# Performance work log

Hardware: AMD Instinct MI355X
Metric: run time of the kernel (lower is better)

## Reference

```python
import jax, jax.numpy as jnp
import numpy as np

NH = 16   # n_heads
HD = 64   # head_size
EMB = 1024  # n_embd = NH * HD
B, T = 4, 2048


def setup_inputs() -> dict:
    key = jax.random.key(0)
    k1, k2, k3 = jax.random.split(key, 3)
    x = jax.random.normal(k1, (B, T, EMB), dtype=jnp.float32)
    # torch Linear(in, out, bias=False): weight [out,in]; we store transposed [in,out]
    W_attn = jax.random.normal(k2, (EMB, 3 * NH * HD), dtype=jnp.float32) * (EMB ** -0.5)
    W_proj = jax.random.normal(k3, (NH * HD, EMB), dtype=jnp.float32) * ((NH * HD) ** -0.5)
    b_proj = jnp.zeros((EMB,), dtype=jnp.float32)
    return {"x": x, "W_attn": W_attn, "W_proj": W_proj, "b_proj": b_proj}


def reference(x, W_attn, W_proj, b_proj):
    Bq, Tq, C = x.shape
    qkv = x @ W_attn                      # [B,T,3*Nh*H]
    qs, ks, vs = jnp.split(qkv, 3, axis=2)
    def to_heads(t):                      # [B,T,Nh*H] -> [B,Nh,T,H]
        return t.reshape(Bq, Tq, NH, HD).transpose(0, 2, 1, 3)
    q, k, v = to_heads(qs), to_heads(ks), to_heads(vs)
    scores = jnp.einsum('bnth,bnsh->bnts', q, k) * (HD ** -0.5)  # [B,Nh,T,T]
    causal = jnp.tril(jnp.ones((Tq, Tq), dtype=bool))
    scores = jnp.where(causal, scores, -jnp.inf)
    attn = jax.nn.softmax(scores, axis=-1)
    # dropout is identity in eval mode
    y = jnp.einsum('bnts,bnsh->bnth', attn, v)                   # [B,Nh,T,H]
    y = y.transpose(0, 2, 1, 3).reshape(Bq, Tq, NH * HD)
    return y @ W_proj + b_proj
```

## Files before the change

kernel.cpp:

```cpp
#include <hip/hip_runtime.h>
#include <hip/hip_bf16.h>

#define NH 16
#define HD 64
#define EMB 1024
#define BB 4
#define TT 2048
#define MTOT (BB*TT)
#define N1 (3*NH*HD)
#define KD EMB

#define QSCALE 0.18033688011112042f
#define FMAX 14.0f

typedef __bf16 bf16x8 __attribute__((ext_vector_type(8)));
typedef __bf16 bf16x4 __attribute__((ext_vector_type(4)));
typedef float  f32x4  __attribute__((ext_vector_type(4)));
typedef __hip_bfloat16 hbf;

__device__ __forceinline__ void async_copy16(const hbf* g, hbf* l) {
    __builtin_amdgcn_global_load_lds(
        (const __attribute__((address_space(1))) void*)g,
        (__attribute__((address_space(3))) void*)l, 16, 0, 0);
}

__device__ __forceinline__ bf16x4 pack4(float x0, float x1, float x2, float x3) {
    union { bf16x4 v; hbf a[4]; } u;
    u.a[0] = __float2bfloat16(x0);
    u.a[1] = __float2bfloat16(x1);
    u.a[2] = __float2bfloat16(x2);
    u.a[3] = __float2bfloat16(x3);
    return u.v;
}


__global__ __launch_bounds__(256) void f32_to_bf16_v4(const float* __restrict__ in,
                                                      hbf* __restrict__ out, int n4) {
    int i = blockIdx.x * blockDim.x + threadIdx.x;
    if (i < n4) {
        float4 v = ((const float4*)in)[i];
        *(bf16x4*)(out + 4 * (size_t)i) = pack4(v.x, v.y, v.z, v.w);
    }
}

__global__ __launch_bounds__(256) void f32_to_bf16_T(const float* __restrict__ in,
                                                     hbf* __restrict__ out, int R, int C) {
    __shared__ float T[64][65];
    int bc = blockIdx.x % (C / 64), br = blockIdx.x / (C / 64);
    int r0 = br * 64, c0 = bc * 64;
    int tr = threadIdx.x >> 6, tc = threadIdx.x & 63;
    #pragma unroll
    for (int i = 0; i < 16; ++i)
        T[4 * i + tr][tc] = in[(size_t)(r0 + 4 * i + tr) * C + c0 + tc];
    __syncthreads();
    #pragma unroll
    for (int i = 0; i < 16; ++i)
        out[(size_t)(c0 + 4 * i + tr) * R + r0 + tc] = __float2bfloat16(T[tc][4 * i + tr]);
}


template<int NBN, int MODE>
__global__ __launch_bounds__(512, 4) void gemm8(
    const hbf* __restrict__ A, const hbf* __restrict__ Bt,
    hbf* __restrict__ qh, hbf* __restrict__ kh, hbf* __restrict__ vt,
    const float* __restrict__ bias, float* __restrict__ out)
{
    constexpr int NKT = KD / 64;
    __shared__ __align__(16) hbf As[2 * 128 * 64];
    __shared__ __align__(16) hbf Bs[2 * 128 * 64];

    int tid = threadIdx.x;
    int wv = tid >> 6, lane = tid & 63;
    int g = lane >> 4, c = lane & 15;
    int wm = wv >> 2, wn = wv & 3;
    int bn = blockIdx.x % NBN, bm = blockIdx.x / NBN;
    int m0 = bm * 128, n0 = bn * 128;

    int sr0 = tid >> 3;
    int sgc = (tid & 7) ^ (sr0 & 7);
    const hbf* Asrc0 = A  + (size_t)(m0 + sr0) * KD + sgc * 8;
    const hbf* Asrc1 = A  + (size_t)(m0 + 64 + sr0) * KD + sgc * 8;
    const hbf* Bsrc0 = Bt + (size_t)(n0 + sr0) * KD + sgc * 8;
    const hbf* Bsrc1 = Bt + (size_t)(n0 + 64 + sr0) * KD + sgc * 8;
    int ldst0 = (tid & ~63) * 8;
    int ldst1 = 4096 + (tid & ~63) * 8;

#define STAGE_A8(tt, buf) { async_copy16(Asrc0 + (tt) * 64, As + (buf) * 8192 + ldst0); \
                            async_copy16(Asrc1 + (tt) * 64, As + (buf) * 8192 + ldst1); }
#define STAGE_B8(tt, buf) { async_copy16(Bsrc0 + (tt) * 64, Bs + (buf) * 8192 + ldst0); \
                            async_copy16(Bsrc1 + (tt) * 64, Bs + (buf) * 8192 + ldst1); }

    int xr = c & 7;
    int aoff0 = (wm * 64 + c) * 64 + ((g ^ xr) << 3);
    int aoff1 = (wm * 64 + c) * 64 + (((4 + g) ^ xr) << 3);
    int boff0 = (wn * 32 + c) * 64 + ((g ^ xr) << 3);
    int boff1 = (wn * 32 + c) * 64 + (((4 + g) ^ xr) << 3);

    f32x4 acc[4][2];
    #pragma unroll
    for (int i = 0; i < 4; ++i)
        #pragma unroll
        for (int j = 0; j < 2; ++j) acc[i][j] = (f32x4){0.f, 0.f, 0.f, 0.f};

    STAGE_A8(0, 0);
    STAGE_B8(0, 0);
    STAGE_A8(1, 1);
    asm volatile("s_waitcnt vmcnt(2)" ::: "memory");
    asm volatile("s_barrier" ::: "memory");
    __builtin_amdgcn_sched_barrier(0);

    for (int t = 0; t < NKT; ++t) {
        int cur = t & 1;
        const hbf* Ab = As + cur * 8192;
        const hbf* Bb = Bs + cur * 8192;
        bf16x8 af[4][2], bfr[2];
        #pragma unroll
        for (int i = 0; i < 4; ++i) {
            af[i][0] = *(const bf16x8*)(Ab + aoff0 + i * 1024);
            af[i][1] = *(const bf16x8*)(Ab + aoff1 + i * 1024);
        }
        bfr[0] = *(const bf16x8*)(Bb + boff0);
        bfr[1] = *(const bf16x8*)(Bb + boff1);
        if (t + 1 < NKT) STAGE_B8(t + 1, cur ^ 1);
        __builtin_amdgcn_s_setprio(1);
        #pragma unroll
        for (int i = 0; i < 4; ++i) {
            acc[i][0] = __builtin_amdgcn_mfma_f32_16x16x32_bf16(af[i][0], bfr[0], acc[i][0], 0, 0, 0);
            acc[i][0] = __builtin_amdgcn_mfma_f32_16x16x32_bf16(af[i][1], bfr[1], acc[i][0], 0, 0, 0);
        }
        __builtin_amdgcn_s_setprio(0);
        asm volatile("s_barrier" ::: "memory");
        __builtin_amdgcn_sched_barrier(0);
        bfr[0] = *(const bf16x8*)(Bb + boff0 + 1024);
        bfr[1] = *(const bf16x8*)(Bb + boff1 + 1024);
        if (t + 2 < NKT) STAGE_A8(t + 2, cur);
        __builtin_amdgcn_s_setprio(1);
        #pragma unroll
        for (int i = 0; i < 4; ++i) {
            acc[i][1] = __builtin_amdgcn_mfma_f32_16x16x32_bf16(af[i][0], bfr[0], acc[i][1], 0, 0, 0);
            acc[i][1] = __builtin_amdgcn_mfma_f32_16x16x32_bf16(af[i][1], bfr[1], acc[i][1], 0, 0, 0);
        }
        __builtin_amdgcn_s_setprio(0);
        if (t + 2 < NKT) { asm volatile("s_waitcnt vmcnt(2)" ::: "memory"); }
        else             { asm volatile("s_waitcnt vmcnt(0)" ::: "memory"); }
        asm volatile("s_barrier" ::: "memory");
        __builtin_amdgcn_sched_barrier(0);
    }

#undef STAGE_A8
#undef STAGE_B8

    if constexpr (MODE == 0) {
        int colbase = n0 + wn * 32;
        int which = colbase >> 10;
        int h = (colbase & 1023) >> 6;
        int dbase = colbase & 63;
        int b = m0 / TT;
        int trow = (m0 % TT) + wm * 64;
        if (which < 2) {
            float scale = (which == 0) ? QSCALE : 1.0f;
            hbf* dst = ((which == 0) ? qh : kh) + ((size_t)b * NH + h) * TT * HD;
            #pragma unroll
            for (int i = 0; i < 4; ++i)
                #pragma unroll
                for (int nf = 0; nf < 2; ++nf) {
                    int d = dbase + nf * 16 + c;
                    #pragma unroll
                    for (int r = 0; r < 4; ++r) {
                        int trw = trow + i * 16 + g * 4 + r;
                        dst[(size_t)trw * HD + d] = __float2bfloat16(acc[i][nf][r] * scale);
                    }
                }
        } else {
            hbf* dst = vt + ((size_t)b * NH + h) * TT * HD;
            #pragma unroll
            for (int i = 0; i < 4; ++i)
                #pragma unroll
                for (int nf = 0; nf < 2; ++nf) {
                    int d = dbase + nf * 16 + c;
                    #pragma unroll
                    for (int r = 0; r < 4; ++r) {
                        int trw = trow + i * 16 + g * 4 + r;
                        dst[(size_t)d * TT + trw] = __float2bfloat16(acc[i][nf][r]);
                    }
                }
        }
    } else {
        #pragma unroll
        for (int i = 0; i < 4; ++i)
            #pragma unroll
            for (int nf = 0; nf < 2; ++nf) {
                int col = n0 + wn * 32 + nf * 16 + c;
                float bv = bias[col];
                #pragma unroll
                for (int r = 0; r < 4; ++r) {
                    int row = m0 + wm * 64 + i * 16 + g * 4 + r;
                    out[(size_t)row * EMB + col] = acc[i][nf][r] + bv;
                }
            }
    }
}


__global__ __launch_bounds__(512, 4) void attn(
    const hbf* __restrict__ qh, const hbf* __restrict__ kh, const hbf* __restrict__ vt,
    hbf* __restrict__ y)
{
    __shared__ __align__(16) hbf Ks[128 * 64];
    __shared__ __align__(16) hbf Vs[64 * 128];
    __shared__ __align__(16) hbf Ps[8][16 * 64];

    int tid = threadIdx.x;
    int wv = tid >> 6, lane = tid & 63;
    int g = lane >> 4, c = lane & 15;
    int c7 = c & 7;

    int bh = blockIdx.x >> 3;
    int pi = blockIdx.x & 7;
    int b = bh >> 4, h = bh & 15;

    const hbf* Q = qh + (size_t)bh * TT * HD;
    const hbf* K = kh + (size_t)bh * TT * HD;
    const hbf* V = vt + (size_t)bh * TT * HD;
    hbf* Pq = &Ps[wv][0];

    union { bf16x8 v; hbf a[8]; } uo;
    #pragma unroll
    for (int i = 0; i < 8; ++i) uo.a[i] = __float2bfloat16(1.0f);
    const bf16x8 ones8 = uo.v;

    #pragma unroll
    for (int pass = 0; pass < 2; ++pass) {
        int sst = pass ? (15 - pi) : pi;
        int qb = sst * 128;
        int q0 = qb + wv * 16;
        int kend = q0 + 16;
        int kmax = qb + 128;

        bf16x8 aq0 = *(const bf16x8*)(Q + (size_t)(q0 + c) * HD + g * 8);
        bf16x8 aq1 = *(const bf16x8*)(Q + (size_t)(q0 + c) * HD + 32 + g * 8);

        f32x4 lacc = (f32x4){0.f, 0.f, 0.f, 0.f};
        f32x4 o[4];
        #pragma unroll
        for (int d = 0; d < 4; ++d) o[d] = (f32x4){0.f, 0.f, 0.f, 0.f};

        for (int k0 = 0; k0 < kmax; k0 += 128) {
            __syncthreads();
            #pragma unroll
            for (int it = 0; it < 2; ++it) {
                int e = it * 4096 + tid * 8;
                int key = e >> 6, sblk = (e >> 3) & 7;
                int dblk = sblk ^ (key & 7);
                async_copy16(K + (size_t)(k0 + key) * HD + dblk * 8,
                             Ks + it * 4096 + (tid & ~63) * 8);
            }
            #pragma unroll
            for (int it = 0; it < 2; ++it) {
                int e = it * 4096 + tid * 8;
                int dim = e >> 7, kb = (e >> 3) & 15;
                int skb = kb ^ (dim & 7);
                async_copy16(V + (size_t)dim * TT + k0 + skb * 8,
                             Vs + it * 4096 + (tid & ~63) * 8);
            }
            __syncthreads();

            #pragma unroll
            for (int ch = 0; ch < 2; ++ch) {
                int c64 = k0 + ch * 64;
                if (c64 < kend) {
                    f32x4 s[4];
                    #pragma unroll
                    for (int t = 0; t < 4; ++t) {
                        int kt = c64 + 16 * t;
                        if (kt < kend) {
                            int rb = (ch * 64 + 16 * t + c) * 64;
                            bf16x8 kf0 = *(const bf16x8*)(Ks + rb + ((g ^ c7) << 3));
                            bf16x8 kf1 = *(const bf16x8*)(Ks + rb + (((4 + g) ^ c7) << 3));
                            f32x4 a = (f32x4){-FMAX, -FMAX, -FMAX, -FMAX};
                            a = __builtin_amdgcn_mfma_f32_16x16x32_bf16(kf0, aq0, a, 0, 0, 0);
                            a = __builtin_amdgcn_mfma_f32_16x16x32_bf16(kf1, aq1, a, 0, 0, 0);
                            if (kt == q0) {
                                #pragma unroll
                                for (int r = 0; r < 4; ++r)
                                    a[r] = (g * 4 + r <= c) ? a[r] : -1e30f;
                            }
                            s[t] = a;
                        } else
                            s[t] = (f32x4){-1e30f, -1e30f, -1e30f, -1e30f};
                    }
                    #pragma unroll
                    for (int t = 0; t < 4; ++t) {
                        f32x4 e;
                        #pragma unroll
                        for (int r = 0; r < 4; ++r) e[r] = __builtin_amdgcn_exp2f(s[t][r]);
                        *(bf16x4*)(Pq + c * 64 + (((2 * t + (g >> 1)) ^ c7) << 3) + ((g & 1) << 2)) =
                            pack4(e[0], e[1], e[2], e[3]);
                    }
                    #pragma unroll
                    for (int sc = 0; sc < 2; ++sc) {
                        if (c64 + 32 * sc < kend) {
                            bf16x8 pf = *(const bf16x8*)(Pq + c * 64 + (((4 * sc + g) ^ c7) << 3));
                            lacc = __builtin_amdgcn_mfma_f32_16x16x32_bf16(ones8, pf, lacc, 0, 0, 0);
                            #pragma unroll
                            for (int d = 0; d < 4; ++d) {
                                int dim = d * 16 + c;
                                bf16x8 vf = *(const bf16x8*)(Vs + dim * 128 +
                                              (((ch * 8 + 4 * sc + g) ^ c7) << 3));
                                o[d] = __builtin_amdgcn_mfma_f32_16x16x32_bf16(vf, pf, o[d], 0, 0, 0);
                            }
                        }
                    }
                }
            }
        }

        float inv = 1.0f / lacc[0];
        #pragma unroll
        for (int d = 0; d < 4; ++d) {
            *(bf16x4*)(y + (size_t)(b * TT + q0 + c) * EMB + h * HD + d * 16 + g * 4) =
                pack4(o[d][0] * inv, o[d][1] * inv, o[d][2] * inv, o[d][3] * inv);
        }
    }
}


extern "C" void kernel_launch(void* const* d_in, const int* in_sizes, int n_in,
                              void* d_out, int out_size, void* d_ws, size_t ws_size,
                              hipStream_t stream)
{
    const float* x      = (const float*)d_in[0];
    const float* W_attn = (const float*)d_in[1];
    const float* W_proj = (const float*)d_in[2];
    const float* b_proj = (const float*)d_in[3];
    float* out = (float*)d_out;

    char* ws = (char*)d_ws;
    hbf* xb    = (hbf*)ws; ws += (size_t)MTOT * KD * 2;
    hbf* wab_t = (hbf*)ws; ws += (size_t)N1 * KD * 2;
    hbf* wpb_t = (hbf*)ws; ws += (size_t)EMB * EMB * 2;
    hbf* qh    = (hbf*)ws; ws += (size_t)MTOT * EMB * 2;
    hbf* kh    = (hbf*)ws; ws += (size_t)MTOT * EMB * 2;
    hbf* vt    = (hbf*)ws; ws += (size_t)MTOT * EMB * 2;
    hbf* yb    = (hbf*)ws; ws += (size_t)MTOT * EMB * 2;

    f32_to_bf16_v4<<<(MTOT * KD / 4 + 255) / 256, 256, 0, stream>>>(x, xb, MTOT * KD / 4);
    f32_to_bf16_T<<<(KD / 64) * (N1 / 64), 256, 0, stream>>>(W_attn, wab_t, KD, N1);
    f32_to_bf16_T<<<(KD / 64) * (EMB / 64), 256, 0, stream>>>(W_proj, wpb_t, KD, EMB);

    gemm8<N1 / 128, 0><<<(MTOT / 128) * (N1 / 128), 512, 0, stream>>>(
        xb, wab_t, qh, kh, vt, nullptr, nullptr);
    attn<<<BB * NH * 8, 512, 0, stream>>>(qh, kh, vt, yb);
    gemm8<EMB / 128, 1><<<(MTOT / 128) * (EMB / 128), 512, 0, stream>>>(
        yb, wpb_t, nullptr, nullptr, nullptr, b_proj, out);
}
```

Measured before the change: 254.2 us.

## Use 256x256 GEMM tiles with ping-pong pipeline and remap block indices

The bf16 GEMM kernels are rewritten to compute 256x256 output tiles per workgroup instead of 128x128. The K loop is restructured into a quarter-tile schedule that interleaves LDS fragment loads, async global-to-LDS staging and MFMA bursts, with explicit barriers and double buffering. Block indices are remapped (XCD-aware) for both the GEMMs and the attention kernel to improve L2 locality. The aim is more data reuse per loaded byte and better overlap of memory with compute. In exchange the kernel uses more LDS and registers per workgroup (occupancy hint reduced to 2) and launches fewer workgroups.

```diff
diff --git a/kernel.cpp b/kernel.cpp
--- a/kernel.cpp
+++ b/kernel.cpp
@@ -59,145 +59,182 @@
 }
 
 
+#define GBAR  asm volatile("s_barrier" ::: "memory")
+#define GLGKM { asm volatile("s_waitcnt lgkmcnt(0)" ::: "memory"); __builtin_amdgcn_sched_barrier(0); }
+
 template<int NBN, int MODE>
-__global__ __launch_bounds__(512, 4) void gemm8(
+__global__ __launch_bounds__(512, 2) void gemm8p(
     const hbf* __restrict__ A, const hbf* __restrict__ Bt,
     hbf* __restrict__ qh, hbf* __restrict__ kh, hbf* __restrict__ vt,
     const float* __restrict__ bias, float* __restrict__ out)
 {
     constexpr int NKT = KD / 64;
-    __shared__ __align__(16) hbf As[2 * 128 * 64];
-    __shared__ __align__(16) hbf Bs[2 * 128 * 64];
+    constexpr int NIT = NKT / 2;
+    constexpr int GRID = (MTOT / 256) * NBN;
+    __shared__ __align__(16) hbf As[2 * 2 * 8192];
+    __shared__ __align__(16) hbf Bs[2 * 2 * 8192];
 
     int tid = threadIdx.x;
     int wv = tid >> 6, lane = tid & 63;
     int g = lane >> 4, c = lane & 15;
     int wm = wv >> 2, wn = wv & 3;
-    int bn = blockIdx.x % NBN, bm = blockIdx.x / NBN;
-    int m0 = bm * 128, n0 = bn * 128;
-
-    int sr0 = tid >> 3;
-    int sgc = (tid & 7) ^ (sr0 & 7);
-    const hbf* Asrc0 = A  + (size_t)(m0 + sr0) * KD + sgc * 8;
-    const hbf* Asrc1 = A  + (size_t)(m0 + 64 + sr0) * KD + sgc * 8;
-    const hbf* Bsrc0 = Bt + (size_t)(n0 + sr0) * KD + sgc * 8;
-    const hbf* Bsrc1 = Bt + (size_t)(n0 + 64 + sr0) * KD + sgc * 8;
-    int ldst0 = (tid & ~63) * 8;
-    int ldst1 = 4096 + (tid & ~63) * 8;
-
-#define STAGE_A8(tt, buf) { async_copy16(Asrc0 + (tt) * 64, As + (buf) * 8192 + ldst0); \
-                            async_copy16(Asrc1 + (tt) * 64, As + (buf) * 8192 + ldst1); }
-#define STAGE_B8(tt, buf) { async_copy16(Bsrc0 + (tt) * 64, Bs + (buf) * 8192 + ldst0); \
-                            async_copy16(Bsrc1 + (tt) * 64, Bs + (buf) * 8192 + ldst1); }
-
     int xr = c & 7;
-    int aoff0 = (wm * 64 + c) * 64 + ((g ^ xr) << 3);
-    int aoff1 = (wm * 64 + c) * 64 + (((4 + g) ^ xr) << 3);
-    int boff0 = (wn * 32 + c) * 64 + ((g ^ xr) << 3);
-    int boff1 = (wn * 32 + c) * 64 + (((4 + g) ^ xr) << 3);
-
-    f32x4 acc[4][2];
-    #pragma unroll
-    for (int i = 0; i < 4; ++i)
+    int wg = (blockIdx.x & 7) * (GRID / 8) + (blockIdx.x >> 3);
+    int bn = wg % NBN, bm = wg / NBN;
+    int m0 = bm * 256, n0 = bn * 256;
+
+    int r0 = tid >> 3;
+    int gc = (tid & 7) ^ (r0 & 7);
+    const hbf* pA = A  + (size_t)(m0 + r0) * KD + gc * 8;
+    const hbf* pB = Bt + (size_t)(n0 + r0) * KD + gc * 8;
+    int ldsd = (tid & ~63) * 8;
+
+#define STG_A(t, buf, hf) { \
+    async_copy16(pA + (size_t)((hf)*128     ) * KD + (t)*64, As + (buf)*16384 + (hf)*8192 + ldsd); \
+    async_copy16(pA + (size_t)((hf)*128 + 64) * KD + (t)*64, As + (buf)*16384 + (hf)*8192 + 4096 + ldsd); }
+#define STG_B(t, buf, hf) { \
+    async_copy16(pB + (size_t)((hf)*128     ) * KD + (t)*64, Bs + (buf)*16384 + (hf)*8192 + ldsd); \
+    async_copy16(pB + (size_t)((hf)*128 + 64) * KD + (t)*64, Bs + (buf)*16384 + (hf)*8192 + 4096 + ldsd); }
+
+    bf16x8 af[4][2];
+    bf16x8 bfr[2][2][2];
+    f32x4 acc[2][2][4][2];
+    #pragma unroll
+    for (int a0 = 0; a0 < 2; ++a0)
+      #pragma unroll
+      for (int a1 = 0; a1 < 2; ++a1)
         #pragma unroll
-        for (int j = 0; j < 2; ++j) acc[i][j] = (f32x4){0.f, 0.f, 0.f, 0.f};
-
-    STAGE_A8(0, 0);
-    STAGE_B8(0, 0);
-    STAGE_A8(1, 1);
-    asm volatile("s_waitcnt vmcnt(2)" ::: "memory");
-    asm volatile("s_barrier" ::: "memory");
+        for (int a2 = 0; a2 < 4; ++a2)
+          #pragma unroll
+          for (int a3 = 0; a3 < 2; ++a3) acc[a0][a1][a2][a3] = (f32x4){0.f,0.f,0.f,0.f};
+
+#define LDA(buf, mh) { _Pragma("unroll") for (int mi = 0; mi < 4; ++mi) { \
+    const hbf* ap = As + (buf)*16384 + wm*8192 + ((mh)*64 + mi*16 + c)*64; \
+    af[mi][0] = *(const bf16x8*)(ap + ((g ^ xr) << 3)); \
+    af[mi][1] = *(const bf16x8*)(ap + (((4 + g) ^ xr) << 3)); } }
+#define LDB(buf, nq) { _Pragma("unroll") for (int ni = 0; ni < 2; ++ni) { \
+    const hbf* bp = Bs + (buf)*16384 + (wn >> 1)*8192 + ((wn & 1)*64 + (nq)*32 + ni*16 + c)*64; \
+    bfr[nq][ni][0] = *(const bf16x8*)(bp + ((g ^ xr) << 3)); \
+    bfr[nq][ni][1] = *(const bf16x8*)(bp + (((4 + g) ^ xr) << 3)); } }
+#define MM(mh, nq) { __builtin_amdgcn_s_setprio(1); \
+    _Pragma("unroll") for (int mi = 0; mi < 4; ++mi) \
+      _Pragma("unroll") for (int ni = 0; ni < 2; ++ni) { \
+        acc[mh][nq][mi][ni] = __builtin_amdgcn_mfma_f32_16x16x32_bf16(af[mi][0], bfr[nq][ni][0], acc[mh][nq][mi][ni], 0, 0, 0); \
+        acc[mh][nq][mi][ni] = __builtin_amdgcn_mfma_f32_16x16x32_bf16(af[mi][1], bfr[nq][ni][1], acc[mh][nq][mi][ni], 0, 0, 0); } \
+    __builtin_amdgcn_s_setprio(0); }
+
+    STG_A(0, 0, 0); STG_A(0, 0, 1); STG_B(0, 0, 0); STG_B(0, 0, 1);
+    STG_B(1, 1, 0); STG_B(1, 1, 1);
+    asm volatile("s_waitcnt vmcnt(4)" ::: "memory");
+    GBAR;
     __builtin_amdgcn_sched_barrier(0);
 
-    for (int t = 0; t < NKT; ++t) {
-        int cur = t & 1;
-        const hbf* Ab = As + cur * 8192;
-        const hbf* Bb = Bs + cur * 8192;
-        bf16x8 af[4][2], bfr[2];
-        #pragma unroll
-        for (int i = 0; i < 4; ++i) {
-            af[i][0] = *(const bf16x8*)(Ab + aoff0 + i * 1024);
-            af[i][1] = *(const bf16x8*)(Ab + aoff1 + i * 1024);
-        }
-        bfr[0] = *(const bf16x8*)(Bb + boff0);
-        bfr[1] = *(const bf16x8*)(Bb + boff1);
-        if (t + 1 < NKT) STAGE_B8(t + 1, cur ^ 1);
-        __builtin_amdgcn_s_setprio(1);
-        #pragma unroll
-        for (int i = 0; i < 4; ++i) {
-            acc[i][0] = __builtin_amdgcn_mfma_f32_16x16x32_bf16(af[i][0], bfr[0], acc[i][0], 0, 0, 0);
-            acc[i][0] = __builtin_amdgcn_mfma_f32_16x16x32_bf16(af[i][1], bfr[1], acc[i][0], 0, 0, 0);
-        }
-        __builtin_amdgcn_s_setprio(0);
-        asm volatile("s_barrier" ::: "memory");
+    for (int i = 0; i < NIT - 1; ++i) {
+        LDA(0, 0); LDB(0, 0); STG_A(2*i+1, 1, 0);
+        GBAR; GLGKM; MM(0, 0); GBAR;
+        LDB(0, 1); STG_A(2*i+1, 1, 1);
+        GBAR; GLGKM; MM(0, 1); GBAR;
+        LDA(0, 1); STG_B(2*i+2, 0, 0);
+        GBAR; GLGKM; MM(1, 0); GBAR;
+        STG_B(2*i+2, 0, 1);
+        GBAR; MM(1, 1);
+        asm volatile("s_waitcnt vmcnt(4)" ::: "memory");
+        GBAR;
+        LDA(1, 0); LDB(1, 0); STG_A(2*i+2, 0, 0);
+        GBAR; GLGKM; MM(0, 0); GBAR;
+        LDB(1, 1); STG_A(2*i+2, 0, 1);
+        GBAR; GLGKM; MM(0, 1); GBAR;
+        LDA(1, 1); STG_B(2*i+3, 1, 0);
+        GBAR; GLGKM; MM(1, 0); GBAR;
+        STG_B(2*i+3, 1, 1);
+        GBAR; MM(1, 1);
+        asm volatile("s_waitcnt vmcnt(4)" ::: "memory");
+        GBAR;
         __builtin_amdgcn_sched_barrier(0);
-        bfr[0] = *(const bf16x8*)(Bb + boff0 + 1024);
-        bfr[1] = *(const bf16x8*)(Bb + boff1 + 1024);
-        if (t + 2 < NKT) STAGE_A8(t + 2, cur);
-        __builtin_amdgcn_s_setprio(1);
-        #pragma unroll
-        for (int i = 0; i < 4; ++i) {
-            acc[i][1] = __builtin_amdgcn_mfma_f32_16x16x32_bf16(af[i][0], bfr[0], acc[i][1], 0, 0, 0);
-            acc[i][1] = __builtin_amdgcn_mfma_f32_16x16x32_bf16(af[i][1], bfr[1], acc[i][1], 0, 0, 0);
-        }
-        __builtin_amdgcn_s_setprio(0);
-        if (t + 2 < NKT) { asm volatile("s_waitcnt vmcnt(2)" ::: "memory"); }
-        else             { asm volatile("s_waitcnt vmcnt(0)" ::: "memory"); }
-        asm volatile("s_barrier" ::: "memory");
-        __builtin_amdgcn_sched_barrier(0);
-    }
-
-#undef STAGE_A8
-#undef STAGE_B8
+    }
+    {
+        LDA(0, 0); LDB(0, 0); STG_A(NKT-1, 1, 0);
+        GBAR; GLGKM; MM(0, 0); GBAR;
+        LDB(0, 1); STG_A(NKT-1, 1, 1);
+        GBAR; GLGKM; MM(0, 1); GBAR;
+        LDA(0, 1);
+        GBAR; GLGKM; MM(1, 0); GBAR;
+        MM(1, 1);
+        asm volatile("s_waitcnt vmcnt(0)" ::: "memory");
+        GBAR;
+        LDA(1, 0); LDB(1, 0);
+        GBAR; GLGKM; MM(0, 0); GBAR;
+        LDB(1, 1);
+        GBAR; GLGKM; MM(0, 1); GBAR;
+        LDA(1, 1);
+        GBAR; GLGKM; MM(1, 0); GBAR;
+        MM(1, 1);
+    }
+#undef STG_A
+#undef STG_B
+#undef LDA
+#undef LDB
+#undef MM
 
     if constexpr (MODE == 0) {
-        int colbase = n0 + wn * 32;
+        int colbase = n0 + wn * 64;
         int which = colbase >> 10;
         int h = (colbase & 1023) >> 6;
-        int dbase = colbase & 63;
         int b = m0 / TT;
-        int trow = (m0 % TT) + wm * 64;
+        int trow0 = (m0 % TT) + wm * 128;
         if (which < 2) {
             float scale = (which == 0) ? QSCALE : 1.0f;
             hbf* dst = ((which == 0) ? qh : kh) + ((size_t)b * NH + h) * TT * HD;
             #pragma unroll
-            for (int i = 0; i < 4; ++i)
+            for (int mh = 0; mh < 2; ++mh)
+              #pragma unroll
+              for (int mi = 0; mi < 4; ++mi)
                 #pragma unroll
-                for (int nf = 0; nf < 2; ++nf) {
-                    int d = dbase + nf * 16 + c;
-                    #pragma unroll
-                    for (int r = 0; r < 4; ++r) {
-                        int trw = trow + i * 16 + g * 4 + r;
-                        dst[(size_t)trw * HD + d] = __float2bfloat16(acc[i][nf][r] * scale);
-                    }
-                }
+                for (int nq = 0; nq < 2; ++nq)
+                  #pragma unroll
+                  for (int ni = 0; ni < 2; ++ni) {
+                      int d = nq * 32 + ni * 16 + c;
+                      #pragma unroll
+                      for (int r = 0; r < 4; ++r) {
+                          int t = trow0 + mh * 64 + mi * 16 + g * 4 + r;
+                          dst[(size_t)t * HD + d] = __float2bfloat16(acc[mh][nq][mi][ni][r] * scale);
+                      }
+                  }
         } else {
             hbf* dst = vt + ((size_t)b * NH + h) * TT * HD;
             #pragma unroll
-            for (int i = 0; i < 4; ++i)
+            for (int mh = 0; mh < 2; ++mh)
+              #pragma unroll
+              for (int mi = 0; mi < 4; ++mi)
                 #pragma unroll
-                for (int nf = 0; nf < 2; ++nf) {
-                    int d = dbase + nf * 16 + c;
-                    #pragma unroll
-                    for (int r = 0; r < 4; ++r) {
-                        int trw = trow + i * 16 + g * 4 + r;
-                        dst[(size_t)d * TT + trw] = __float2bfloat16(acc[i][nf][r]);
-                    }
-                }
+                for (int nq = 0; nq < 2; ++nq)
+                  #pragma unroll
+                  for (int ni = 0; ni < 2; ++ni) {
+                      int d = nq * 32 + ni * 16 + c;
+                      #pragma unroll
+                      for (int r = 0; r < 4; ++r) {
+                          int t = trow0 + mh * 64 + mi * 16 + g * 4 + r;
+                          dst[(size_t)d * TT + t] = __float2bfloat16(acc[mh][nq][mi][ni][r]);
+                      }
+                  }
         }
     } else {
         #pragma unroll
-        for (int i = 0; i < 4; ++i)
-            #pragma unroll
-            for (int nf = 0; nf < 2; ++nf) {
-                int col = n0 + wn * 32 + nf * 16 + c;
-                float bv = bias[col];
-                #pragma unroll
-                for (int r = 0; r < 4; ++r) {
-                    int row = m0 + wm * 64 + i * 16 + g * 4 + r;
-                    out[(size_t)row * EMB + col] = acc[i][nf][r] + bv;
-                }
-            }
+        for (int mh = 0; mh < 2; ++mh)
+          #pragma unroll
+          for (int mi = 0; mi < 4; ++mi)
+            #pragma unroll
+            for (int nq = 0; nq < 2; ++nq)
+              #pragma unroll
+              for (int ni = 0; ni < 2; ++ni) {
+                  int col = n0 + wn * 64 + nq * 32 + ni * 16 + c;
+                  float bv = bias[col];
+                  #pragma unroll
+                  for (int r = 0; r < 4; ++r) {
+                      int row = m0 + wm * 128 + mh * 64 + mi * 16 + g * 4 + r;
+                      out[(size_t)row * EMB + col] = acc[mh][nq][mi][ni][r] + bv;
+                  }
+              }
     }
 }
 
@@ -215,8 +252,9 @@
     int g = lane >> 4, c = lane & 15;
     int c7 = c & 7;
 
-    int bh = blockIdx.x >> 3;
-    int pi = blockIdx.x & 7;
+    int bidx = blockIdx.x;
+    int bh = (bidx & 7) | (((bidx >> 6) & 7) << 3);
+    int pi = (bidx >> 3) & 7;
     int b = bh >> 4, h = bh & 15;
 
     const hbf* Q = qh + (size_t)bh * TT * HD;
@@ -348,9 +386,9 @@
     f32_to_bf16_T<<<(KD / 64) * (N1 / 64), 256, 0, stream>>>(W_attn, wab_t, KD, N1);
     f32_to_bf16_T<<<(KD / 64) * (EMB / 64), 256, 0, stream>>>(W_proj, wpb_t, KD, EMB);
 
-    gemm8<N1 / 128, 0><<<(MTOT / 128) * (N1 / 128), 512, 0, stream>>>(
+    gemm8p<N1 / 256, 0><<<(MTOT / 256) * (N1 / 256), 512, 0, stream>>>(
         xb, wab_t, qh, kh, vt, nullptr, nullptr);
     attn<<<BB * NH * 8, 512, 0, stream>>>(qh, kh, vt, yb);
-    gemm8<EMB / 128, 1><<<(MTOT / 128) * (EMB / 128), 512, 0, stream>>>(
+    gemm8p<EMB / 256, 1><<<(MTOT / 256) * (EMB / 256), 512, 0, stream>>>(
         yb, wpb_t, nullptr, nullptr, nullptr, b_proj, out);
 }
```

Result: slower. 270.6 us (+6.4%).
